# Kernel optimization log

Measured on AMD Instinct MI355X. Metric: run time of the kernel, lower is better.

## Reference

```python
import jax, jax.numpy as jnp
import numpy as np

TOP_K = 4  # num_experts_per_tok


def setup_inputs() -> dict:
    key = jax.random.key(0)
    ks = jax.random.split(key, 8)
    B, S, H, E, F = 1, 2048, 2048, 16, 1408
    Fs = 2 * F  # shared expert intermediate = moe_intermediate_size * n_shared_experts
    s = 0.02  # weight init scale for sane numerics
    return {
        "hidden_states": jax.random.normal(ks[0], (B, S, H), jnp.float32),
        "gate_weight": jax.random.normal(ks[1], (E, H), jnp.float32) * s,
        "w_gate": jax.random.normal(ks[2], (E, H, F), jnp.float32) * s,
        "w_up": jax.random.normal(ks[3], (E, H, F), jnp.float32) * s,
        "w_down": jax.random.normal(ks[4], (E, F, H), jnp.float32) * s,
        "ws_gate": jax.random.normal(ks[5], (H, Fs), jnp.float32) * s,
        "ws_up": jax.random.normal(ks[6], (H, Fs), jnp.float32) * s,
        "ws_down": jax.random.normal(ks[7], (Fs, H), jnp.float32) * s,
    }


def reference(hidden_states, gate_weight, w_gate, w_up, w_down, ws_gate, ws_up, ws_down):
    B, S, H = hidden_states.shape
    E = gate_weight.shape[0]
    x = hidden_states.reshape(-1, H)  # [T, H]
    T = x.shape[0]

    # --- gate: fp32 linear, softmax over experts, top-k, scatter to dense mask ---
    logits = jnp.einsum("th,eh->te", x.astype(jnp.float32), gate_weight.astype(jnp.float32))
    probs = jax.nn.softmax(logits, axis=1)
    top_vals, top_idx = jax.lax.top_k(probs, TOP_K)  # [T, K]
    # dense routing weights [T, E]; scatter_add of top-k softmax values (no renorm)
    dense_w = jnp.zeros((T, E), probs.dtype).at[jnp.arange(T)[:, None], top_idx].add(top_vals)

    # --- routed experts: gated SiLU MLP per expert, weighted combine ---
    g = jnp.einsum("th,ehf->tef", x, w_gate)
    u = jnp.einsum("th,ehf->tef", x, w_up)
    a = jax.nn.silu(g) * u  # [T, E, F]
    # fold expert combine into the down projection to avoid a [T, E, H] intermediate
    routed = jnp.einsum("te,tef,efh->th", dense_w.astype(x.dtype), a, w_down)

    # --- shared expert on identity path ---
    shared = jnp.einsum("tf,fh->th", jax.nn.silu(x @ ws_gate) * (x @ ws_up), ws_down)

    out = (routed + shared).reshape(B, S, H)
    return out
```

## Files before the change

kernel.cpp:

```cpp
#include <hip/hip_runtime.h>

#define TT 2048
#define HD 2048
#define FD 1408
#define NE 16
#define NG 18

typedef __attribute__((ext_vector_type(4))) float f32x4;
typedef __attribute__((ext_vector_type(8))) short short8;
typedef __attribute__((ext_vector_type(8))) __bf16 bf16x8;
typedef __attribute__((ext_vector_type(4))) unsigned short u16x4;
typedef __attribute__((ext_vector_type(8))) unsigned short u16x8;

__device__ __forceinline__ unsigned short f2bf(float f) {
  unsigned u = __builtin_bit_cast(unsigned, f);
  u += 0x7fffu + ((u >> 16) & 1u);
  return (unsigned short)(u >> 16);
}

template <typename T>
__device__ __forceinline__ auto mfma_try(T a, T b, f32x4 c, int)
    -> decltype(__builtin_amdgcn_mfma_f32_16x16x32_bf16(a, b, c, 0, 0, 0)) {
  return __builtin_amdgcn_mfma_f32_16x16x32_bf16(a, b, c, 0, 0, 0);
}
template <typename T, typename BV = bf16x8>
__device__ __forceinline__ f32x4 mfma_try(T a, T b, f32x4 c, long) {
  BV aa = __builtin_bit_cast(BV, a);
  BV bb = __builtin_bit_cast(BV, b);
  return __builtin_amdgcn_mfma_f32_16x16x32_bf16(aa, bb, c, 0, 0, 0);
}
__device__ __forceinline__ f32x4 mfma16(short8 a, short8 b, f32x4 c) {
  return mfma_try(a, b, c, 0);
}

__device__ __forceinline__ void gload16(const void* g, void* l) {
  __builtin_amdgcn_global_load_lds(
      (const __attribute__((address_space(1))) void*)g,
      (__attribute__((address_space(3))) void*)l, 16, 0, 0);
}

__global__ void gate_kernel(const float* __restrict__ x, const float* __restrict__ gw,
                            float* __restrict__ dense_w) {
  int wid = threadIdx.x >> 6;
  int lane = threadIdx.x & 63;
  int t = blockIdx.x * 4 + wid;
  if (t >= TT) return;
  const float* xr = x + (size_t)t * HD;
  float acc[NE];
#pragma unroll
  for (int e = 0; e < NE; ++e) acc[e] = 0.f;
  for (int h = lane; h < HD; h += 64) {
    float xv = xr[h];
#pragma unroll
    for (int e = 0; e < NE; ++e) acc[e] += xv * gw[e * HD + h];
  }
#pragma unroll
  for (int e = 0; e < NE; ++e) {
    float v = acc[e];
#pragma unroll
    for (int s = 32; s > 0; s >>= 1) v += __shfl_xor(v, s, 64);
    acc[e] = v;
  }
  float mx = acc[0];
#pragma unroll
  for (int e = 1; e < NE; ++e) mx = fmaxf(mx, acc[e]);
  float p[NE]; float sum = 0.f;
#pragma unroll
  for (int e = 0; e < NE; ++e) { p[e] = __expf(acc[e] - mx); sum += p[e]; }
  float inv = 1.f / sum;
#pragma unroll
  for (int e = 0; e < NE; ++e) p[e] *= inv;
  unsigned chosen = 0;
#pragma unroll
  for (int k = 0; k < 4; ++k) {
    int bi = 0; float bv = -1.f;
#pragma unroll
    for (int e = 0; e < NE; ++e) {
      bool ok = !((chosen >> e) & 1) && (p[e] > bv);
      bv = ok ? p[e] : bv;
      bi = ok ? e : bi;
    }
    chosen |= 1u << bi;
  }
  if (lane < NE)
    dense_w[t * NE + lane] = ((chosen >> lane) & 1) ? p[lane] : 0.f;
}

__global__ void build_lists(const float* __restrict__ dense_w, int* __restrict__ tok,
                            float* __restrict__ scale, int* __restrict__ counts) {
  int g = blockIdx.x;
  int lane = threadIdx.x;
  if (g >= NE) {
    for (int i = lane; i < TT; i += 64) { tok[g * TT + i] = i; scale[g * TT + i] = 1.f; }
    if (lane == 0) counts[g] = TT;
    return;
  }
  int base = 0;
  for (int c0 = 0; c0 < TT; c0 += 64) {
    int t = c0 + lane;
    float w = dense_w[t * NE + g];
    bool pred = w > 0.f;
    unsigned long long b = __ballot(pred);
    if (pred) {
      int pos = base + __popcll(b & ((1ull << lane) - 1ull));
      tok[g * TT + pos] = t;
      scale[g * TT + pos] = w;
    }
    base += __popcll(b);
  }
  if (lane == 0) counts[g] = base;
}

__global__ void prefix_kernel(const int* __restrict__ counts, int* __restrict__ rowOff) {
  if (threadIdx.x == 0) {
    int s = 0;
    for (int g = 0; g < NE; ++g) { rowOff[g] = s; s += counts[g]; }
    rowOff[16] = 4 * TT;
    rowOff[17] = 4 * TT + TT;
  }
}

__global__ void cvt_bf16_kernel(const float* __restrict__ in,
                                unsigned short* __restrict__ out, int n4) {
  int i = blockIdx.x * blockDim.x + threadIdx.x;
  if (i < n4) {
    f32x4 v = ((const f32x4*)in)[i];
    u16x4 h;
    h.x = f2bf(v.x); h.y = f2bf(v.y); h.z = f2bf(v.z); h.w = f2bf(v.w);
    ((u16x4*)out)[i] = h;
  }
}

__global__ __launch_bounds__(256) void transpose_bf16_kernel(
    const float* __restrict__ in, unsigned short* __restrict__ out, int R, int C) {
  __shared__ float tile[64 * 65];
  const size_t base = (size_t)blockIdx.z * R * C;
  const int c0 = blockIdx.x * 64, r0 = blockIdx.y * 64;
  const int tid = threadIdx.x;
  const int rr = tid >> 4;
  const int c4 = (tid & 15) * 4;
#pragma unroll
  for (int it = 0; it < 4; ++it) {
    int r = rr + it * 16;
    f32x4 v = *(const f32x4*)(in + base + (size_t)(r0 + r) * C + c0 + c4);
#pragma unroll
    for (int i = 0; i < 4; ++i) tile[(c4 + i) * 65 + r] = v[i];
  }
  __syncthreads();
  const int cl = tid >> 3;
  const int rc = (tid & 7) * 8;
#pragma unroll
  for (int it = 0; it < 2; ++it) {
    int c = cl + it * 32;
    u16x8 h;
#pragma unroll
    for (int j = 0; j < 8; ++j) h[j] = f2bf(tile[c * 65 + rc + j]);
    *(u16x8*)(out + base + (size_t)(c0 + c) * R + r0 + rc) = h;
  }
}

#define CB1 (FD / 64)
#define NPAN1 (CB1 * NG)
#define PG1 ((NPAN1 + 7) / 8)

__global__ __launch_bounds__(256, 4) void gemm1_v5(
    const unsigned short* __restrict__ xb,
    const unsigned short* __restrict__ wgT, const unsigned short* __restrict__ wuT,
    const unsigned short* __restrict__ wsgT, const unsigned short* __restrict__ wsuT,
    const int* __restrict__ tok, const float* __restrict__ scale,
    const int* __restrict__ counts, const int* __restrict__ rowOff,
    unsigned short* __restrict__ Abuf) {
  const int b = blockIdx.x;
  const int xcd = b & 7;
  const int s_ = b >> 3;
  const int rb = s_ & 15;
  const int panel = (s_ >> 4) * 8 + xcd;
  if (panel >= NPAN1) return;
  const int g = panel / CB1, cb = panel % CB1;
  const int count = counts[g];
  if (rb * 128 >= count) return;

  __shared__ __align__(16) unsigned short sA[2][128 * 32];
  __shared__ __align__(16) unsigned short sG[2][64 * 32];
  __shared__ __align__(16) unsigned short sU[2][64 * 32];

  const int tid = threadIdx.x, lane = tid & 63, wid = tid >> 6;
  const int wr = (wid >> 1) * 64, wc = (wid & 1) * 32;

  const int lr = lane >> 2, lc = lane & 3;
  const int ra0 = wid * 32 + lr, ra1 = wid * 32 + 16 + lr;
  int gi0 = rb * 128 + ra0, gi1 = rb * 128 + ra1;
  int t0 = (gi0 < count) ? tok[g * TT + gi0] : 0;
  int t1 = (gi1 < count) ? tok[g * TT + gi1] : 0;
  const unsigned short* aG0 = xb + (size_t)t0 * HD + ((lc ^ ((ra0 >> 1) & 3)) * 8);
  const unsigned short* aG1 = xb + (size_t)t1 * HD + ((lc ^ ((ra1 >> 1) & 3)) * 8);
  const int rbb = wid * 16 + lr;
  const unsigned short *bGg, *bGu;
  if (g < NE) {
    size_t o = (size_t)g * FD * HD + (size_t)(cb * 64 + rbb) * HD;
    bGg = wgT + o; bGu = wuT + o;
  } else {
    size_t o = (size_t)((g - NE) * FD + cb * 64 + rbb) * HD;
    bGg = wsgT + o; bGu = wsuT + o;
  }
  const int bco = (lc ^ ((rbb >> 1) & 3)) * 8;
  bGg += bco; bGu += bco;

  const f32x4 fz = {0.f, 0.f, 0.f, 0.f};
  f32x4 accg[4][2], accu[4][2];
#pragma unroll
  for (int m = 0; m < 4; ++m)
#pragma unroll
    for (int n = 0; n < 2; ++n) { accg[m][n] = fz; accu[m][n] = fz; }

  auto STAGE = [&](int bu, int s) {
    size_t ko = (size_t)s * 32;
    gload16(aG0 + ko, &sA[bu][wid * 1024 + lr * 32]);
    gload16(aG1 + ko, &sA[bu][wid * 1024 + 512 + lr * 32]);
    gload16(bGg + ko, &sG[bu][wid * 512 + lr * 32]);
    gload16(bGu + ko, &sU[bu][wid * 512 + lr * 32]);
  };
  auto STAGEW = [&](int bu, int s) {
    size_t ko = (size_t)s * 32;
    gload16(aG0 + ko, &sA[bu][wid * 1024]);
    gload16(aG1 + ko, &sA[bu][wid * 1024 + 512]);
    gload16(bGg + ko, &sG[bu][wid * 512]);
    gload16(bGu + ko, &sU[bu][wid * 512]);
  };
  (void)STAGE;

  auto COMPUTE = [&](int bu) {
    const int ksel = lane >> 4;
    short8 av[4], bg[2], bv[2];
#pragma unroll
    for (int n = 0; n < 2; ++n) {
      int c = wc + n * 16 + (lane & 15);
      int idx = c * 32 + ((ksel ^ ((c >> 1) & 3)) << 3);
      bg[n] = *(const short8*)&sG[bu][idx];
      bv[n] = *(const short8*)&sU[bu][idx];
    }
#pragma unroll
    for (int m = 0; m < 4; ++m) {
      int r = wr + m * 16 + (lane & 15);
      av[m] = *(const short8*)&sA[bu][r * 32 + ((ksel ^ ((r >> 1) & 3)) << 3)];
    }
#pragma unroll
    for (int m = 0; m < 4; ++m)
#pragma unroll
      for (int n = 0; n < 2; ++n) {
        accg[m][n] = mfma16(av[m], bg[n], accg[m][n]);
        accu[m][n] = mfma16(av[m], bv[n], accu[m][n]);
      }
  };

  const int NK = HD / 32;
  STAGEW(0, 0);
  __syncthreads();
  int bu = 0;
#pragma unroll 1
  for (int s = 0; s < NK; ++s) {
    if (s + 1 < NK) STAGEW(bu ^ 1, s + 1);
    COMPUTE(bu);
    __syncthreads();
    bu ^= 1;
  }

  const int rowBase = rowOff[g] + rb * 128;
#pragma unroll
  for (int m = 0; m < 4; ++m)
#pragma unroll
    for (int r = 0; r < 4; ++r) {
      int rl = wr + m * 16 + ((lane >> 4) << 2) + r;
      int gi = rb * 128 + rl;
      if (gi < count) {
        float sc = scale[g * TT + gi];
#pragma unroll
        for (int n = 0; n < 2; ++n) {
          int cl = wc + n * 16 + (lane & 15);
          float gv = accg[m][n][r], uv = accu[m][n][r];
          float a = gv / (1.f + __expf(-gv)) * uv * sc;
          Abuf[(size_t)(rowBase + rl) * FD + cb * 64 + cl] = f2bf(a);
        }
      }
    }
}

#define CB2 (HD / 128)
#define NPAN2 (CB2 * NG)
#define PG2 (NPAN2 / 8)

__global__ __launch_bounds__(256, 4) void gemm2_v5(
    const unsigned short* __restrict__ Abuf,
    const unsigned short* __restrict__ wdT, const unsigned short* __restrict__ wsdT,
    const int* __restrict__ tok, const int* __restrict__ counts,
    const int* __restrict__ rowOff, float* __restrict__ out) {
  const int b = blockIdx.x;
  const int xcd = b & 7;
  const int s_ = b >> 3;
  const int rb = s_ & 15;
  const int panel = (s_ >> 4) * 8 + xcd;
  if (panel >= NPAN2) return;
  const int g = panel / CB2, cb = panel % CB2;
  const int count = counts[g];
  if (rb * 128 >= count) return;

  __shared__ __align__(16) unsigned short sA[2][128 * 32];
  __shared__ __align__(16) unsigned short sB[2][128 * 32];

  const int tid = threadIdx.x, lane = tid & 63, wid = tid >> 6;
  const int wr = (wid >> 1) * 64, wc = (wid & 1) * 64;

  const int rowBase = rowOff[g] + rb * 128;

  const int lr = lane >> 2, lc = lane & 3;
  const int ra0 = wid * 32 + lr, ra1 = wid * 32 + 16 + lr;
  const unsigned short* aG0 =
      Abuf + (size_t)(rowBase + ra0) * FD + ((lc ^ ((ra0 >> 1) & 3)) * 8);
  const unsigned short* aG1 =
      Abuf + (size_t)(rowBase + ra1) * FD + ((lc ^ ((ra1 >> 1) & 3)) * 8);
  const int rb0 = wid * 32 + lr, rb1 = wid * 32 + 16 + lr;
  const unsigned short *bG0, *bG1;
  if (g < NE) {
    bG0 = wdT + (size_t)g * HD * FD + (size_t)(cb * 128 + rb0) * FD;
    bG1 = wdT + (size_t)g * HD * FD + (size_t)(cb * 128 + rb1) * FD;
  } else {
    bG0 = wsdT + (size_t)(cb * 128 + rb0) * (2 * FD) + (size_t)(g - NE) * FD;
    bG1 = wsdT + (size_t)(cb * 128 + rb1) * (2 * FD) + (size_t)(g - NE) * FD;
  }
  bG0 += (lc ^ ((rb0 >> 1) & 3)) * 8;
  bG1 += (lc ^ ((rb1 >> 1) & 3)) * 8;

  const f32x4 fz = {0.f, 0.f, 0.f, 0.f};
  f32x4 acc[4][4];
#pragma unroll
  for (int m = 0; m < 4; ++m)
#pragma unroll
    for (int n = 0; n < 4; ++n) acc[m][n] = fz;

  auto STAGEW = [&](int bu, int s) {
    size_t ko = (size_t)s * 32;
    gload16(aG0 + ko, &sA[bu][wid * 1024]);
    gload16(aG1 + ko, &sA[bu][wid * 1024 + 512]);
    gload16(bG0 + ko, &sB[bu][wid * 1024]);
    gload16(bG1 + ko, &sB[bu][wid * 1024 + 512]);
  };

  auto COMPUTE = [&](int bu) {
    const int ksel = lane >> 4;
    short8 av[4], bv[4];
#pragma unroll
    for (int n = 0; n < 4; ++n) {
      int c = wc + n * 16 + (lane & 15);
      bv[n] = *(const short8*)&sB[bu][c * 32 + ((ksel ^ ((c >> 1) & 3)) << 3)];
    }
#pragma unroll
    for (int m = 0; m < 4; ++m) {
      int r = wr + m * 16 + (lane & 15);
      av[m] = *(const short8*)&sA[bu][r * 32 + ((ksel ^ ((r >> 1) & 3)) << 3)];
    }
#pragma unroll
    for (int m = 0; m < 4; ++m)
#pragma unroll
      for (int n = 0; n < 4; ++n) acc[m][n] = mfma16(av[m], bv[n], acc[m][n]);
  };

  const int NK = FD / 32;
  STAGEW(0, 0);
  __syncthreads();
  int bu = 0;
#pragma unroll 1
  for (int s = 0; s < NK; ++s) {
    if (s + 1 < NK) STAGEW(bu ^ 1, s + 1);
    COMPUTE(bu);
    __syncthreads();
    bu ^= 1;
  }

#pragma unroll
  for (int m = 0; m < 4; ++m)
#pragma unroll
    for (int r = 0; r < 4; ++r) {
      int rl = wr + m * 16 + ((lane >> 4) << 2) + r;
      int gi = rb * 128 + rl;
      if (gi < count) {
        int t = tok[g * TT + gi];
        float* op = out + (size_t)t * HD + cb * 128;
#pragma unroll
        for (int n = 0; n < 4; ++n)
          atomicAdd(op + wc + n * 16 + (lane & 15), acc[m][n][r]);
      }
    }
}

extern "C" void kernel_launch(void* const* d_in, const int* in_sizes, int n_in,
                              void* d_out, int out_size, void* d_ws, size_t ws_size,
                              hipStream_t stream) {
  const float* x      = (const float*)d_in[0];
  const float* gw     = (const float*)d_in[1];
  const float* w_gate = (const float*)d_in[2];
  const float* w_up   = (const float*)d_in[3];
  const float* w_down = (const float*)d_in[4];
  const float* wsg    = (const float*)d_in[5];
  const float* wsu    = (const float*)d_in[6];
  const float* wsd    = (const float*)d_in[7];
  float* out = (float*)d_out;

  char* ws = (char*)d_ws;
  float* dense_w = (float*)(ws);
  int*   tok     = (int*)(ws + (140 << 10));
  float* scale   = (float*)(ws + (290 << 10));
  int*   counts  = (int*)(ws + (440 << 10));
  int*   rowOff  = (int*)(ws + (441 << 10));
  unsigned short* Abuf = (unsigned short*)(ws + (1ull  << 20));
  unsigned short* xb   = (unsigned short*)(ws + (36ull << 20));
  unsigned short* wgT  = (unsigned short*)(ws + (44ull  << 20));
  unsigned short* wuT  = (unsigned short*)(ws + (137ull << 20));
  unsigned short* wdT  = (unsigned short*)(ws + (230ull << 20));
  unsigned short* wsgT = (unsigned short*)(ws + (323ull << 20));
  unsigned short* wsuT = (unsigned short*)(ws + (335ull << 20));
  unsigned short* wsdT = (unsigned short*)(ws + (347ull << 20));

  hipMemsetAsync(d_out, 0, (size_t)out_size * sizeof(float), stream);
  gate_kernel<<<TT / 4, 256, 0, stream>>>(x, gw, dense_w);
  build_lists<<<NG, 64, 0, stream>>>(dense_w, tok, scale, counts);
  prefix_kernel<<<1, 64, 0, stream>>>(counts, rowOff);
  cvt_bf16_kernel<<<(TT * HD / 4 + 255) / 256, 256, 0, stream>>>(x, xb, TT * HD / 4);
  transpose_bf16_kernel<<<dim3(FD / 64, HD / 64, NE), 256, 0, stream>>>(w_gate, wgT, HD, FD);
  transpose_bf16_kernel<<<dim3(FD / 64, HD / 64, NE), 256, 0, stream>>>(w_up,   wuT, HD, FD);
  transpose_bf16_kernel<<<dim3(HD / 64, FD / 64, NE), 256, 0, stream>>>(w_down, wdT, FD, HD);
  transpose_bf16_kernel<<<dim3(2 * FD / 64, HD / 64, 1), 256, 0, stream>>>(wsg, wsgT, HD, 2 * FD);
  transpose_bf16_kernel<<<dim3(2 * FD / 64, HD / 64, 1), 256, 0, stream>>>(wsu, wsuT, HD, 2 * FD);
  transpose_bf16_kernel<<<dim3(HD / 64, 2 * FD / 64, 1), 256, 0, stream>>>(wsd, wsdT, 2 * FD, HD);

  gemm1_v5<<<8 * PG1 * 16, 256, 0, stream>>>(
      xb, wgT, wuT, wsgT, wsuT, tok, scale, counts, rowOff, Abuf);
  gemm2_v5<<<8 * PG2 * 16, 256, 0, stream>>>(
      Abuf, wdT, wsdT, tok, counts, rowOff, out);
}
```

Before: 602.7 us.

## Triple-buffer LDS staging in both expert GEMMs with one barrier per k-step

Both grouped GEMM kernels move from double to triple buffering of their LDS tiles. Two stages are prefetched up front, and the loop uses an explicit vmcnt wait plus a single s_barrier per iteration instead of two __syncthreads. The goal is to hide more global-load latency and halve barrier overhead. In exchange it uses more LDS per block, and launch bounds drop from 4 to 3 blocks per SIMD, which may reduce occupancy.

Result: slower. 619.8 us (+2.9%).

```diff
diff --git a/kernel.cpp b/kernel.cpp
--- a/kernel.cpp
+++ b/kernel.cpp
@@ -163,7 +163,7 @@
 #define NPAN1 (CB1 * NG)
 #define PG1 ((NPAN1 + 7) / 8)
 
-__global__ __launch_bounds__(256, 4) void gemm1_v5(
+__global__ __launch_bounds__(256, 3) void gemm1_v6(
     const unsigned short* __restrict__ xb,
     const unsigned short* __restrict__ wgT, const unsigned short* __restrict__ wuT,
     const unsigned short* __restrict__ wsgT, const unsigned short* __restrict__ wsuT,
@@ -180,9 +180,9 @@
   const int count = counts[g];
   if (rb * 128 >= count) return;
 
-  __shared__ __align__(16) unsigned short sA[2][128 * 32];
-  __shared__ __align__(16) unsigned short sG[2][64 * 32];
-  __shared__ __align__(16) unsigned short sU[2][64 * 32];
+  __shared__ __align__(16) unsigned short sA[3][128 * 32];
+  __shared__ __align__(16) unsigned short sG[3][64 * 32];
+  __shared__ __align__(16) unsigned short sU[3][64 * 32];
 
   const int tid = threadIdx.x, lane = tid & 63, wid = tid >> 6;
   const int wr = (wid >> 1) * 64, wc = (wid & 1) * 32;
@@ -213,13 +213,6 @@
 #pragma unroll
     for (int n = 0; n < 2; ++n) { accg[m][n] = fz; accu[m][n] = fz; }
 
-  auto STAGE = [&](int bu, int s) {
-    size_t ko = (size_t)s * 32;
-    gload16(aG0 + ko, &sA[bu][wid * 1024 + lr * 32]);
-    gload16(aG1 + ko, &sA[bu][wid * 1024 + 512 + lr * 32]);
-    gload16(bGg + ko, &sG[bu][wid * 512 + lr * 32]);
-    gload16(bGu + ko, &sU[bu][wid * 512 + lr * 32]);
-  };
   auto STAGEW = [&](int bu, int s) {
     size_t ko = (size_t)s * 32;
     gload16(aG0 + ko, &sA[bu][wid * 1024]);
@@ -227,7 +220,6 @@
     gload16(bGg + ko, &sG[bu][wid * 512]);
     gload16(bGu + ko, &sU[bu][wid * 512]);
   };
-  (void)STAGE;
 
   auto COMPUTE = [&](int bu) {
     const int ksel = lane >> 4;
@@ -255,14 +247,14 @@
 
   const int NK = HD / 32;
   STAGEW(0, 0);
-  __syncthreads();
-  int bu = 0;
+  STAGEW(1, 1);
 #pragma unroll 1
   for (int s = 0; s < NK; ++s) {
-    if (s + 1 < NK) STAGEW(bu ^ 1, s + 1);
-    COMPUTE(bu);
-    __syncthreads();
-    bu ^= 1;
+    if (s + 1 < NK) asm volatile("s_waitcnt vmcnt(4)" ::: "memory");
+    else            asm volatile("s_waitcnt vmcnt(0)" ::: "memory");
+    __builtin_amdgcn_s_barrier();
+    if (s + 2 < NK) STAGEW((s + 2) % 3, s + 2);
+    COMPUTE(s % 3);
   }
 
   const int rowBase = rowOff[g] + rb * 128;
@@ -289,7 +281,7 @@
 #define NPAN2 (CB2 * NG)
 #define PG2 (NPAN2 / 8)
 
-__global__ __launch_bounds__(256, 4) void gemm2_v5(
+__global__ __launch_bounds__(256, 3) void gemm2_v6(
     const unsigned short* __restrict__ Abuf,
     const unsigned short* __restrict__ wdT, const unsigned short* __restrict__ wsdT,
     const int* __restrict__ tok, const int* __restrict__ counts,
@@ -304,8 +296,8 @@
   const int count = counts[g];
   if (rb * 128 >= count) return;
 
-  __shared__ __align__(16) unsigned short sA[2][128 * 32];
-  __shared__ __align__(16) unsigned short sB[2][128 * 32];
+  __shared__ __align__(16) unsigned short sA[3][128 * 32];
+  __shared__ __align__(16) unsigned short sB[3][128 * 32];
 
   const int tid = threadIdx.x, lane = tid & 63, wid = tid >> 6;
   const int wr = (wid >> 1) * 64, wc = (wid & 1) * 64;
@@ -366,14 +358,14 @@
 
   const int NK = FD / 32;
   STAGEW(0, 0);
-  __syncthreads();
-  int bu = 0;
+  STAGEW(1, 1);
 #pragma unroll 1
   for (int s = 0; s < NK; ++s) {
-    if (s + 1 < NK) STAGEW(bu ^ 1, s + 1);
-    COMPUTE(bu);
-    __syncthreads();
-    bu ^= 1;
+    if (s + 1 < NK) asm volatile("s_waitcnt vmcnt(4)" ::: "memory");
+    else            asm volatile("s_waitcnt vmcnt(0)" ::: "memory");
+    __builtin_amdgcn_s_barrier();
+    if (s + 2 < NK) STAGEW((s + 2) % 3, s + 2);
+    COMPUTE(s % 3);
   }
 
 #pragma unroll
@@ -432,8 +424,8 @@
   transpose_bf16_kernel<<<dim3(2 * FD / 64, HD / 64, 1), 256, 0, stream>>>(wsu, wsuT, HD, 2 * FD);
   transpose_bf16_kernel<<<dim3(HD / 64, 2 * FD / 64, 1), 256, 0, stream>>>(wsd, wsdT, 2 * FD, HD);
 
-  gemm1_v5<<<8 * PG1 * 16, 256, 0, stream>>>(
+  gemm1_v6<<<8 * PG1 * 16, 256, 0, stream>>>(
       xb, wgT, wuT, wsgT, wsuT, tok, scale, counts, rowOff, Abuf);
-  gemm2_v5<<<8 * PG2 * 16, 256, 0, stream>>>(
+  gemm2_v6<<<8 * PG2 * 16, 256, 0, stream>>>(
       Abuf, wdT, wsdT, tok, counts, rowOff, out);
 }
```

## Schedule grouped GEMM tiles from a compacted device-built work list

Applied to the files above, without the earlier changes.

The prefix kernel now builds compact work lists of (group, column block, row block) tiles covering only populated row blocks, plus tile counts in a meta buffer. Both grouped GEMMs launch a fixed upper-bound grid and read their tile from the list, instead of launching all 16 row blocks per panel and early-exiting the empty ones. This removes the many idle blocks in the launch and changes how tiles are spread across XCDs. The cost is an extra indirection and a serial per-thread fill loop in the prefix kernel.

Result: faster. 582.0 us (-3.4%).

```diff
diff --git a/kernel.cpp b/kernel.cpp
--- a/kernel.cpp
+++ b/kernel.cpp
@@ -38,6 +38,11 @@
       (const __attribute__((address_space(1))) void*)g,
       (__attribute__((address_space(3))) void*)l, 16, 0, 0);
 }
+
+#define CB1 (FD / 64)
+#define CB2 (HD / 128)
+#define MAXW1 2464
+#define MAXW2 1792
 
 __global__ void gate_kernel(const float* __restrict__ x, const float* __restrict__ gw,
                             float* __restrict__ dense_w) {
@@ -111,12 +116,36 @@
   if (lane == 0) counts[g] = base;
 }
 
-__global__ void prefix_kernel(const int* __restrict__ counts, int* __restrict__ rowOff) {
-  if (threadIdx.x == 0) {
+__global__ void prefix_kernel(const int* __restrict__ counts, int* __restrict__ rowOff,
+                              int* __restrict__ work1, int* __restrict__ work2,
+                              int* __restrict__ meta) {
+  const int tid = threadIdx.x;
+  auto NRB = [&](int g) { return (counts[g] + 127) >> 7; };
+  if (tid == 0) {
     int s = 0;
     for (int g = 0; g < NE; ++g) { rowOff[g] = s; s += counts[g]; }
     rowOff[16] = 4 * TT;
     rowOff[17] = 4 * TT + TT;
+    int n1 = 0, n2 = 0;
+    for (int g = 0; g < NG; ++g) { n1 += NRB(g) * CB1; n2 += NRB(g) * CB2; }
+    meta[0] = n1; meta[1] = (n1 + 7) / 8;
+    meta[2] = n2; meta[3] = (n2 + 7) / 8;
+  }
+  if (tid < NG * CB1) {
+    int g = tid / CB1, cb = tid % CB1;
+    int base = 0;
+    for (int gg = 0; gg < g; ++gg) base += NRB(gg) * CB1;
+    int n = NRB(g);
+    base += cb * n;
+    for (int r = 0; r < n; ++r) work1[base + r] = (g << 16) | (cb << 8) | r;
+  }
+  if (tid < NG * CB2) {
+    int g = tid / CB2, cb = tid % CB2;
+    int base = 0;
+    for (int gg = 0; gg < g; ++gg) base += NRB(gg) * CB2;
+    int n = NRB(g);
+    base += cb * n;
+    for (int r = 0; r < n; ++r) work2[base + r] = (g << 16) | (cb << 8) | r;
   }
 }
 
@@ -159,26 +188,22 @@
   }
 }
 
-#define CB1 (FD / 64)
-#define NPAN1 (CB1 * NG)
-#define PG1 ((NPAN1 + 7) / 8)
-
-__global__ __launch_bounds__(256, 4) void gemm1_v5(
+__global__ __launch_bounds__(256, 4) void gemm1_v7(
     const unsigned short* __restrict__ xb,
     const unsigned short* __restrict__ wgT, const unsigned short* __restrict__ wuT,
     const unsigned short* __restrict__ wsgT, const unsigned short* __restrict__ wsuT,
     const int* __restrict__ tok, const float* __restrict__ scale,
     const int* __restrict__ counts, const int* __restrict__ rowOff,
+    const int* __restrict__ work, const int* __restrict__ meta,
     unsigned short* __restrict__ Abuf) {
-  const int b = blockIdx.x;
-  const int xcd = b & 7;
-  const int s_ = b >> 3;
-  const int rb = s_ & 15;
-  const int panel = (s_ >> 4) * 8 + xcd;
-  if (panel >= NPAN1) return;
-  const int g = panel / CB1, cb = panel % CB1;
+  const int nw = meta[0], per = meta[1];
+  const int xcd = blockIdx.x & 7, slot = blockIdx.x >> 3;
+  if (slot >= per) return;
+  const int w = xcd * per + slot;
+  if (w >= nw) return;
+  const int e = work[w];
+  const int g = e >> 16, cb = (e >> 8) & 255, rb = e & 255;
   const int count = counts[g];
-  if (rb * 128 >= count) return;
 
   __shared__ __align__(16) unsigned short sA[2][128 * 32];
   __shared__ __align__(16) unsigned short sG[2][64 * 32];
@@ -213,13 +238,6 @@
 #pragma unroll
     for (int n = 0; n < 2; ++n) { accg[m][n] = fz; accu[m][n] = fz; }
 
-  auto STAGE = [&](int bu, int s) {
-    size_t ko = (size_t)s * 32;
-    gload16(aG0 + ko, &sA[bu][wid * 1024 + lr * 32]);
-    gload16(aG1 + ko, &sA[bu][wid * 1024 + 512 + lr * 32]);
-    gload16(bGg + ko, &sG[bu][wid * 512 + lr * 32]);
-    gload16(bGu + ko, &sU[bu][wid * 512 + lr * 32]);
-  };
   auto STAGEW = [&](int bu, int s) {
     size_t ko = (size_t)s * 32;
     gload16(aG0 + ko, &sA[bu][wid * 1024]);
@@ -227,7 +245,6 @@
     gload16(bGg + ko, &sG[bu][wid * 512]);
     gload16(bGu + ko, &sU[bu][wid * 512]);
   };
-  (void)STAGE;
 
   auto COMPUTE = [&](int bu) {
     const int ksel = lane >> 4;
@@ -285,24 +302,20 @@
     }
 }
 
-#define CB2 (HD / 128)
-#define NPAN2 (CB2 * NG)
-#define PG2 (NPAN2 / 8)
-
-__global__ __launch_bounds__(256, 4) void gemm2_v5(
+__global__ __launch_bounds__(256, 4) void gemm2_v7(
     const unsigned short* __restrict__ Abuf,
     const unsigned short* __restrict__ wdT, const unsigned short* __restrict__ wsdT,
     const int* __restrict__ tok, const int* __restrict__ counts,
-    const int* __restrict__ rowOff, float* __restrict__ out) {
-  const int b = blockIdx.x;
-  const int xcd = b & 7;
-  const int s_ = b >> 3;
-  const int rb = s_ & 15;
-  const int panel = (s_ >> 4) * 8 + xcd;
-  if (panel >= NPAN2) return;
-  const int g = panel / CB2, cb = panel % CB2;
+    const int* __restrict__ rowOff, const int* __restrict__ work,
+    const int* __restrict__ meta, float* __restrict__ out) {
+  const int nw = meta[2], per = meta[3];
+  const int xcd = blockIdx.x & 7, slot = blockIdx.x >> 3;
+  if (slot >= per) return;
+  const int w = xcd * per + slot;
+  if (w >= nw) return;
+  const int e = work[w];
+  const int g = e >> 16, cb = (e >> 8) & 255, rb = e & 255;
   const int count = counts[g];
-  if (rb * 128 >= count) return;
 
   __shared__ __align__(16) unsigned short sA[2][128 * 32];
   __shared__ __align__(16) unsigned short sB[2][128 * 32];
@@ -411,6 +424,9 @@
   float* scale   = (float*)(ws + (290 << 10));
   int*   counts  = (int*)(ws + (440 << 10));
   int*   rowOff  = (int*)(ws + (441 << 10));
+  int*   work1   = (int*)(ws + (444 << 10));
+  int*   work2   = (int*)(ws + (456 << 10));
+  int*   meta    = (int*)(ws + (464 << 10));
   unsigned short* Abuf = (unsigned short*)(ws + (1ull  << 20));
   unsigned short* xb   = (unsigned short*)(ws + (36ull << 20));
   unsigned short* wgT  = (unsigned short*)(ws + (44ull  << 20));
@@ -423,7 +439,7 @@
   hipMemsetAsync(d_out, 0, (size_t)out_size * sizeof(float), stream);
   gate_kernel<<<TT / 4, 256, 0, stream>>>(x, gw, dense_w);
   build_lists<<<NG, 64, 0, stream>>>(dense_w, tok, scale, counts);
-  prefix_kernel<<<1, 64, 0, stream>>>(counts, rowOff);
+  prefix_kernel<<<1, 512, 0, stream>>>(counts, rowOff, work1, work2, meta);
   cvt_bf16_kernel<<<(TT * HD / 4 + 255) / 256, 256, 0, stream>>>(x, xb, TT * HD / 4);
   transpose_bf16_kernel<<<dim3(FD / 64, HD / 64, NE), 256, 0, stream>>>(w_gate, wgT, HD, FD);
   transpose_bf16_kernel<<<dim3(FD / 64, HD / 64, NE), 256, 0, stream>>>(w_up,   wuT, HD, FD);
@@ -432,8 +448,8 @@
   transpose_bf16_kernel<<<dim3(2 * FD / 64, HD / 64, 1), 256, 0, stream>>>(wsu, wsuT, HD, 2 * FD);
   transpose_bf16_kernel<<<dim3(HD / 64, 2 * FD / 64, 1), 256, 0, stream>>>(wsd, wsdT, 2 * FD, HD);
 
-  gemm1_v5<<<8 * PG1 * 16, 256, 0, stream>>>(
-      xb, wgT, wuT, wsgT, wsuT, tok, scale, counts, rowOff, Abuf);
-  gemm2_v5<<<8 * PG2 * 16, 256, 0, stream>>>(
-      Abuf, wdT, wsdT, tok, counts, rowOff, out);
-}
+  gemm1_v7<<<MAXW1, 256, 0, stream>>>(
+      xb, wgT, wuT, wsgT, wsuT, tok, scale, counts, rowOff, work1, meta, Abuf);
+  gemm2_v7<<<MAXW2, 256, 0, stream>>>(
+      Abuf, wdT, wsdT, tok, counts, rowOff, work2, meta, out);
+}
```
